# Kernel optimization log

Measured on AMD Instinct MI355X. Metric: run time of the kernel, lower is better.

Reference implementation:

```python
import jax, jax.numpy as jnp
import numpy as np

DIM = 768
H = 4
D_H = DIM // H          # 192
R_H = 16 // H           # 4  (max(1, rank//num_heads))
N_EXP = 6
TOPK = 3
BETA = 0.5
BATCH = 65536


def setup_inputs() -> dict:
    key = jax.random.key(0)
    k_z, k_a, k_b, k_zs, k_za = jax.random.split(key, 5)
    z = jax.random.normal(k_z, (BATCH, DIM), dtype=jnp.float32)
    A = jax.random.normal(k_a, (N_EXP, D_H, R_H), dtype=jnp.float32) * 0.02
    B = jax.random.normal(k_b, (N_EXP, R_H, D_H), dtype=jnp.float32) * 0.02
    Z_share = jax.random.normal(k_zs, (H, N_EXP), dtype=jnp.float32) * 0.02
    Z_auth = jax.random.normal(k_za, (H, N_EXP), dtype=jnp.float32) * 0.02
    return {"z": z, "A": A, "B": B, "Z_share": Z_share, "Z_auth": Z_auth}


def _route(z_heads, Z_router, A, B):
    # z_heads: [Bt, h, d_h]; Z_router: [h, E]
    probs = jax.nn.softmax(Z_router, axis=-1)            # [h, E]
    top_vals, top_idx = jax.lax.top_k(probs, TOPK)       # [h, k]
    w = top_vals / (jnp.sum(top_vals, axis=-1, keepdims=True) + 1e-8)  # renorm per head
    A_g = A[top_idx]                                     # [h, k, d_h, r_h]
    B_g = B[top_idx]                                     # [h, k, r_h, d_h]
    # tmp[b,h,k,r] = z[b,h,:] @ A_g[h,k]
    tmp = jnp.einsum('bhd,hkdr->bhkr', z_heads, A_g)
    delta = jnp.einsum('bhkr,hkrd,hk->bhd', tmp, B_g, w)
    return delta


def reference(z, A, B, Z_share, Z_auth):
    Bt = z.shape[0]
    z_heads = z.reshape(Bt, H, D_H)
    delta = _route(z_heads, Z_share, A, B) + _route(z_heads, Z_auth, A, B)
    return z + BETA * delta.reshape(Bt, DIM)
```

## Files before the change

kernel.cpp:

```cpp
#include <hip/hip_runtime.h>
#include <hip/hip_bf16.h>


typedef float f4 __attribute__((ext_vector_type(4)));
typedef unsigned int u32;
typedef u32 u32x4 __attribute__((ext_vector_type(4)));

__device__ __forceinline__ u32 pack_bf16(float a, float b) {
  const u32 ua = __builtin_bit_cast(u32, a) + 0x8000u;
  const u32 ub = __builtin_bit_cast(u32, b) + 0x8000u;
  return (ua >> 16) | (ub & 0xFFFF0000u);
}

#if __has_builtin(__builtin_amdgcn_fdot2_f32_bf16)
typedef __bf16 bf16x2 __attribute__((ext_vector_type(2)));
__device__ __forceinline__ float dot2(u32 a, u32 b, float c) {
  return __builtin_amdgcn_fdot2_f32_bf16(__builtin_bit_cast(bf16x2, a),
                                         __builtin_bit_cast(bf16x2, b), c, false);
}
#else
__device__ __forceinline__ float dot2(u32 a, u32 b, float c) {
  const float alo = __builtin_bit_cast(float, a << 16);
  const float ahi = __builtin_bit_cast(float, a & 0xFFFF0000u);
  const float blo = __builtin_bit_cast(float, b << 16);
  const float bhi = __builtin_bit_cast(float, b & 0xFFFF0000u);
  return fmaf(ahi, bhi, fmaf(alo, blo, c));
}
#endif

__global__ void dff_setup(const float* __restrict__ A,
                          const float* __restrict__ Bm,
                          const float* __restrict__ Zs,
                          const float* __restrict__ Za,
                          u32* __restrict__ T) {
  __shared__ float c[4][6];
  const int t = threadIdx.x;
  if (t < 4) {
    const int h = t;
    float cc[6] = {0.f, 0.f, 0.f, 0.f, 0.f, 0.f};
    for (int rt = 0; rt < 2; ++rt) {
      const float* Z = rt ? Za : Zs;
      float zz[6];
      float mx = -1e30f;
      for (int e = 0; e < 6; ++e) { zz[e] = Z[h * 6 + e]; mx = fmaxf(mx, zz[e]); }
      float p[6];
      float sum = 0.f;
      for (int e = 0; e < 6; ++e) { p[e] = expf(zz[e] - mx); sum += p[e]; }
      for (int e = 0; e < 6; ++e) p[e] /= sum;
      bool used[6] = {false, false, false, false, false, false};
      float ws = 0.f;
      int sel[3];
      float pv[3];
      for (int k = 0; k < 3; ++k) {
        int best = -1;
        float bv = -1.f;
        for (int e = 0; e < 6; ++e)
          if (!used[e] && p[e] > bv) { bv = p[e]; best = e; }
        used[best] = true;
        sel[k] = best;
        pv[k] = bv;
        ws += bv;
      }
      const float inv = 1.f / (ws + 1e-8f);
      for (int k = 0; k < 3; ++k) cc[sel[k]] += pv[k] * inv;
    }
    for (int e = 0; e < 6; ++e) c[h][e] = 0.5f * cc[e];
  }
  __syncthreads();
  for (int i = threadIdx.x; i < 11520; i += blockDim.x) {
    if (i < 9216) {
      const int h = i / 2304;
      const int rem = i % 2304;
      const int s = rem / 96;
      const int dp = rem % 96;
      const int e = s >> 2, r = s & 3;
      const float lo = c[h][e] * A[e * 768 + (2 * dp) * 4 + r];
      const float hi = c[h][e] * A[e * 768 + (2 * dp + 1) * 4 + r];
      T[i] = pack_bf16(lo, hi);
    } else {
      const int k = i - 9216;
      const int sp = k / 192;
      const int d = k % 192;
      T[i] = pack_bf16(Bm[(2 * sp) * 192 + d], Bm[(2 * sp + 1) * 192 + d]);
    }
  }
}

__global__ __launch_bounds__(256, 4)
void dff_main(const float* __restrict__ z,
              const u32* __restrict__ T,
              float* __restrict__ out) {
  __shared__ __align__(16) u32 sT[4608];
  u32x4* sT4 = reinterpret_cast<u32x4*>(sT);

  const int t = threadIdx.x;
  const int q = t & 7;
  const int rl = t >> 3;
  const int h = blockIdx.y;
  const int row = blockIdx.x * 32 + rl;
  const float* __restrict__ zp = z + (size_t)row * 768 + h * 192;
  float* __restrict__ op = out + (size_t)row * 768 + h * 192;

  f4 zv[6];
#pragma unroll
  for (int k = 0; k < 6; ++k)
    zv[k] = reinterpret_cast<const f4*>(zp)[16 * (k >> 1) + 2 * q + (k & 1)];

  {
    const u32x4* __restrict__ Tw = reinterpret_cast<const u32x4*>(T);
    for (int i = t; i < 576; i += 256) {
      sT4[i] = Tw[h * 576 + i];
      sT4[576 + i] = Tw[2304 + i];
    }
  }

  u32 zpk[12];
#pragma unroll
  for (int j = 0; j < 3; ++j) {
    zpk[4 * j + 0] = pack_bf16(zv[2 * j].x, zv[2 * j].y);
    zpk[4 * j + 1] = pack_bf16(zv[2 * j].z, zv[2 * j].w);
    zpk[4 * j + 2] = pack_bf16(zv[2 * j + 1].x, zv[2 * j + 1].y);
    zpk[4 * j + 3] = pack_bf16(zv[2 * j + 1].z, zv[2 * j + 1].w);
  }
  __syncthreads();

  float tmp[24];
#pragma unroll
  for (int s = 0; s < 24; ++s) {
    float acc = 0.f;
#pragma unroll
    for (int j = 0; j < 3; ++j) {
      const u32x4 av = sT4[s * 24 + 8 * j + q];
      acc = dot2(zpk[4 * j + 0], av.x, acc);
      acc = dot2(zpk[4 * j + 1], av.y, acc);
      acc = dot2(zpk[4 * j + 2], av.z, acc);
      acc = dot2(zpk[4 * j + 3], av.w, acc);
    }
    tmp[s] = acc;
  }

#pragma unroll
  for (int s = 0; s < 24; ++s) {
    tmp[s] += __shfl_xor(tmp[s], 1, 64);
    tmp[s] += __shfl_xor(tmp[s], 2, 64);
    tmp[s] += __shfl_xor(tmp[s], 4, 64);
  }

  u32 tp[12];
#pragma unroll
  for (int i = 0; i < 12; ++i) tp[i] = pack_bf16(tmp[2 * i], tmp[2 * i + 1]);

#pragma unroll
  for (int j = 0; j < 3; ++j) {
    const int c0 = 16 * j + 2 * q;
    f4 o0 = reinterpret_cast<const f4*>(zp)[c0];
    f4 o1 = reinterpret_cast<const f4*>(zp)[c0 + 1];
#pragma unroll
    for (int sp = 0; sp < 12; ++sp) {
      const int base = 576 + sp * 48 + (8 * j + q) * 2;
      const u32x4 b0 = sT4[base];
      const u32x4 b1 = sT4[base + 1];
      o0.x = dot2(tp[sp], b0.x, o0.x);
      o0.y = dot2(tp[sp], b0.y, o0.y);
      o0.z = dot2(tp[sp], b0.z, o0.z);
      o0.w = dot2(tp[sp], b0.w, o0.w);
      o1.x = dot2(tp[sp], b1.x, o1.x);
      o1.y = dot2(tp[sp], b1.y, o1.y);
      o1.z = dot2(tp[sp], b1.z, o1.z);
      o1.w = dot2(tp[sp], b1.w, o1.w);
    }
    __builtin_nontemporal_store(o0, reinterpret_cast<f4*>(op) + c0);
    __builtin_nontemporal_store(o1, reinterpret_cast<f4*>(op) + c0 + 1);
  }
}

extern "C" void kernel_launch(void* const* d_in, const int* in_sizes, int n_in,
                              void* d_out, int out_size, void* d_ws, size_t ws_size,
                              hipStream_t stream) {
  const float* z  = (const float*)d_in[0];
  const float* A  = (const float*)d_in[1];
  const float* Bm = (const float*)d_in[2];
  const float* Zs = (const float*)d_in[3];
  const float* Za = (const float*)d_in[4];
  float* out = (float*)d_out;
  u32* T = (u32*)d_ws;

  dff_setup<<<1, 256, 0, stream>>>(A, Bm, Zs, Za, T);
  dff_main<<<dim3(2048, 4), 256, 0, stream>>>(z, T, out);
}
```

Before: 133.1 us.

## Process two rows per thread, DPP reductions, and plain stores

Each thread now handles two rows, 32 apart, so every LDS read of the A and B tables is reused across both rows, and the grid is halved. The shuffle-based 8-lane reduction is replaced with DPP quad-permute and ds_swizzle operations. The stage-one loop is chunked so that reduction and packing interleave. Output stores change from nontemporal to ordinary stores. This reduces LDS traffic and per-block table loading but doubles register pressure under launch_bounds(256,4), which may cost occupancy.

```diff
diff --git a/kernel.cpp b/kernel.cpp
--- a/kernel.cpp
+++ b/kernel.cpp
@@ -27,6 +27,18 @@
   return fmaf(ahi, bhi, fmaf(alo, blo, c));
 }
 #endif
+
+__device__ __forceinline__ float qsum8(float x) {
+  int xi = __builtin_bit_cast(int, x);
+  x += __builtin_bit_cast(float,
+        __builtin_amdgcn_update_dpp(0, xi, 0xB1, 0xF, 0xF, true));
+  xi = __builtin_bit_cast(int, x);
+  x += __builtin_bit_cast(float,
+        __builtin_amdgcn_update_dpp(0, xi, 0x4E, 0xF, 0xF, true));
+  xi = __builtin_bit_cast(int, x);
+  x += __builtin_bit_cast(float, __builtin_amdgcn_ds_swizzle(xi, 0x101F));
+  return x;
+}
 
 __global__ void dff_setup(const float* __restrict__ A,
                           const float* __restrict__ Bm,
@@ -97,14 +109,19 @@
   const int q = t & 7;
   const int rl = t >> 3;
   const int h = blockIdx.y;
-  const int row = blockIdx.x * 32 + rl;
-  const float* __restrict__ zp = z + (size_t)row * 768 + h * 192;
-  float* __restrict__ op = out + (size_t)row * 768 + h * 192;
-
-  f4 zv[6];
-#pragma unroll
-  for (int k = 0; k < 6; ++k)
-    zv[k] = reinterpret_cast<const f4*>(zp)[16 * (k >> 1) + 2 * q + (k & 1)];
+  const int row0 = blockIdx.x * 64 + rl;
+  const float* __restrict__ zp0 = z + (size_t)row0 * 768 + h * 192;
+  const float* __restrict__ zp1 = zp0 + 32 * 768;
+  float* __restrict__ op0 = out + (size_t)row0 * 768 + h * 192;
+  float* __restrict__ op1 = op0 + 32 * 768;
+
+  f4 zv0[6], zv1[6];
+#pragma unroll
+  for (int k = 0; k < 6; ++k) {
+    const int ci = 16 * (k >> 1) + 2 * q + (k & 1);
+    zv0[k] = reinterpret_cast<const f4*>(zp0)[ci];
+    zv1[k] = reinterpret_cast<const f4*>(zp1)[ci];
+  }
 
   {
     const u32x4* __restrict__ Tw = reinterpret_cast<const u32x4*>(T);
@@ -114,63 +131,87 @@
     }
   }
 
-  u32 zpk[12];
+  u32 zpk0[12], zpk1[12];
 #pragma unroll
   for (int j = 0; j < 3; ++j) {
-    zpk[4 * j + 0] = pack_bf16(zv[2 * j].x, zv[2 * j].y);
-    zpk[4 * j + 1] = pack_bf16(zv[2 * j].z, zv[2 * j].w);
-    zpk[4 * j + 2] = pack_bf16(zv[2 * j + 1].x, zv[2 * j + 1].y);
-    zpk[4 * j + 3] = pack_bf16(zv[2 * j + 1].z, zv[2 * j + 1].w);
+    zpk0[4 * j + 0] = pack_bf16(zv0[2 * j].x, zv0[2 * j].y);
+    zpk0[4 * j + 1] = pack_bf16(zv0[2 * j].z, zv0[2 * j].w);
+    zpk0[4 * j + 2] = pack_bf16(zv0[2 * j + 1].x, zv0[2 * j + 1].y);
+    zpk0[4 * j + 3] = pack_bf16(zv0[2 * j + 1].z, zv0[2 * j + 1].w);
+    zpk1[4 * j + 0] = pack_bf16(zv1[2 * j].x, zv1[2 * j].y);
+    zpk1[4 * j + 1] = pack_bf16(zv1[2 * j].z, zv1[2 * j].w);
+    zpk1[4 * j + 2] = pack_bf16(zv1[2 * j + 1].x, zv1[2 * j + 1].y);
+    zpk1[4 * j + 3] = pack_bf16(zv1[2 * j + 1].z, zv1[2 * j + 1].w);
   }
   __syncthreads();
 
-  float tmp[24];
-#pragma unroll
-  for (int s = 0; s < 24; ++s) {
-    float acc = 0.f;
-#pragma unroll
-    for (int j = 0; j < 3; ++j) {
-      const u32x4 av = sT4[s * 24 + 8 * j + q];
-      acc = dot2(zpk[4 * j + 0], av.x, acc);
-      acc = dot2(zpk[4 * j + 1], av.y, acc);
-      acc = dot2(zpk[4 * j + 2], av.z, acc);
-      acc = dot2(zpk[4 * j + 3], av.w, acc);
-    }
-    tmp[s] = acc;
-  }
-
-#pragma unroll
-  for (int s = 0; s < 24; ++s) {
-    tmp[s] += __shfl_xor(tmp[s], 1, 64);
-    tmp[s] += __shfl_xor(tmp[s], 2, 64);
-    tmp[s] += __shfl_xor(tmp[s], 4, 64);
-  }
-
-  u32 tp[12];
-#pragma unroll
-  for (int i = 0; i < 12; ++i) tp[i] = pack_bf16(tmp[2 * i], tmp[2 * i + 1]);
+  u32 tp0[12], tp1[12];
+#pragma unroll
+  for (int c = 0; c < 6; ++c) {
+    float tmp0[4], tmp1[4];
+#pragma unroll
+    for (int u = 0; u < 4; ++u) {
+      const int s = 4 * c + u;
+      float a0 = 0.f, a1 = 0.f;
+#pragma unroll
+      for (int j = 0; j < 3; ++j) {
+        const u32x4 av = sT4[s * 24 + 8 * j + q];
+        a0 = dot2(zpk0[4 * j + 0], av.x, a0);
+        a0 = dot2(zpk0[4 * j + 1], av.y, a0);
+        a0 = dot2(zpk0[4 * j + 2], av.z, a0);
+        a0 = dot2(zpk0[4 * j + 3], av.w, a0);
+        a1 = dot2(zpk1[4 * j + 0], av.x, a1);
+        a1 = dot2(zpk1[4 * j + 1], av.y, a1);
+        a1 = dot2(zpk1[4 * j + 2], av.z, a1);
+        a1 = dot2(zpk1[4 * j + 3], av.w, a1);
+      }
+      tmp0[u] = a0;
+      tmp1[u] = a1;
+    }
+#pragma unroll
+    for (int u = 0; u < 4; ++u) {
+      tmp0[u] = qsum8(tmp0[u]);
+      tmp1[u] = qsum8(tmp1[u]);
+    }
+    tp0[2 * c + 0] = pack_bf16(tmp0[0], tmp0[1]);
+    tp0[2 * c + 1] = pack_bf16(tmp0[2], tmp0[3]);
+    tp1[2 * c + 0] = pack_bf16(tmp1[0], tmp1[1]);
+    tp1[2 * c + 1] = pack_bf16(tmp1[2], tmp1[3]);
+  }
 
 #pragma unroll
   for (int j = 0; j < 3; ++j) {
     const int c0 = 16 * j + 2 * q;
-    f4 o0 = reinterpret_cast<const f4*>(zp)[c0];
-    f4 o1 = reinterpret_cast<const f4*>(zp)[c0 + 1];
+    f4 o00 = reinterpret_cast<const f4*>(zp0)[c0];
+    f4 o01 = reinterpret_cast<const f4*>(zp0)[c0 + 1];
+    f4 o10 = reinterpret_cast<const f4*>(zp1)[c0];
+    f4 o11 = reinterpret_cast<const f4*>(zp1)[c0 + 1];
 #pragma unroll
     for (int sp = 0; sp < 12; ++sp) {
       const int base = 576 + sp * 48 + (8 * j + q) * 2;
       const u32x4 b0 = sT4[base];
       const u32x4 b1 = sT4[base + 1];
-      o0.x = dot2(tp[sp], b0.x, o0.x);
-      o0.y = dot2(tp[sp], b0.y, o0.y);
-      o0.z = dot2(tp[sp], b0.z, o0.z);
-      o0.w = dot2(tp[sp], b0.w, o0.w);
-      o1.x = dot2(tp[sp], b1.x, o1.x);
-      o1.y = dot2(tp[sp], b1.y, o1.y);
-      o1.z = dot2(tp[sp], b1.z, o1.z);
-      o1.w = dot2(tp[sp], b1.w, o1.w);
-    }
-    __builtin_nontemporal_store(o0, reinterpret_cast<f4*>(op) + c0);
-    __builtin_nontemporal_store(o1, reinterpret_cast<f4*>(op) + c0 + 1);
+      o00.x = dot2(tp0[sp], b0.x, o00.x);
+      o00.y = dot2(tp0[sp], b0.y, o00.y);
+      o00.z = dot2(tp0[sp], b0.z, o00.z);
+      o00.w = dot2(tp0[sp], b0.w, o00.w);
+      o01.x = dot2(tp0[sp], b1.x, o01.x);
+      o01.y = dot2(tp0[sp], b1.y, o01.y);
+      o01.z = dot2(tp0[sp], b1.z, o01.z);
+      o01.w = dot2(tp0[sp], b1.w, o01.w);
+      o10.x = dot2(tp1[sp], b0.x, o10.x);
+      o10.y = dot2(tp1[sp], b0.y, o10.y);
+      o10.z = dot2(tp1[sp], b0.z, o10.z);
+      o10.w = dot2(tp1[sp], b0.w, o10.w);
+      o11.x = dot2(tp1[sp], b1.x, o11.x);
+      o11.y = dot2(tp1[sp], b1.y, o11.y);
+      o11.z = dot2(tp1[sp], b1.z, o11.z);
+      o11.w = dot2(tp1[sp], b1.w, o11.w);
+    }
+    reinterpret_cast<f4*>(op0)[c0] = o00;
+    reinterpret_cast<f4*>(op0)[c0 + 1] = o01;
+    reinterpret_cast<f4*>(op1)[c0] = o10;
+    reinterpret_cast<f4*>(op1)[c0 + 1] = o11;
   }
 }
 
@@ -186,5 +227,5 @@
   u32* T = (u32*)d_ws;
 
   dff_setup<<<1, 256, 0, stream>>>(A, Bm, Zs, Za, T);
-  dff_main<<<dim3(2048, 4), 256, 0, stream>>>(z, T, out);
-}
+  dff_main<<<dim3(1024, 4), 256, 0, stream>>>(z, T, out);
+}
```

Measured after the change: 124.9 us. -6.2%, faster.
